# Optimization experiments

Measured on AMD Instinct MI355X. Metric: run time of the kernel, lower is better.

The kernel has to match this reference:

```python
import jax, jax.numpy as jnp
import numpy as np
import math

B, S, D, H = 4, 2048, 1024, 16
HD = D // H
EPS = 1e-10


def setup_inputs() -> dict:
    key = jax.random.key(0)
    kx, kq, kk, kv, ko = jax.random.split(key, 5)
    x = jax.random.normal(kx, (B, S, D), dtype=jnp.float32)
    # causal additive mask: 0 on/below diagonal, -1e9 above
    mask = jnp.where(jnp.triu(jnp.ones((S, S), dtype=bool), k=1), -1e9, 0.0).astype(jnp.float32)
    scale = 1.0 / math.sqrt(D)
    Wq = jax.random.normal(kq, (D, D), dtype=jnp.float32) * scale
    Wk = jax.random.normal(kk, (D, D), dtype=jnp.float32) * scale
    Wv = jax.random.normal(kv, (D, D), dtype=jnp.float32) * scale
    Wo = jax.random.normal(ko, (D, D), dtype=jnp.float32) * scale
    return {"x": x, "mask": mask, "Wq": Wq, "Wk": Wk, "Wv": Wv, "Wo": Wo}


def _nirmalya_softmax(t):
    # faithful to original: plain exp (no max-subtraction), eps in denominator
    p1 = jnp.exp(t)
    return p1 / (jnp.sum(p1, axis=-1, keepdims=True) + EPS)


def reference(x, mask, Wq, Wk, Wv, Wo):
    b, s, d = x.shape
    # torch Linear (bias=False): y = x @ W.T
    def proj(W):
        y = jnp.einsum('bsd,ed->bse', x, W)
        return y.reshape(b, s, H, HD).transpose(0, 2, 1, 3)  # [b,h,s,hd]
    q, k, v = proj(Wq), proj(Wk), proj(Wv)
    scores = jnp.einsum('bhqd,bhkd->bhqk', q, k) / math.sqrt(HD)
    scores = scores + mask  # broadcast over batch/heads
    attn = _nirmalya_softmax(scores)
    out = jnp.einsum('bhqk,bhkd->bhqd', attn, v)
    out = out.transpose(0, 2, 1, 3).reshape(b, s, d)
    return jnp.einsum('bsd,ed->bse', out, Wo)
```

## Files before the change

### kernel.cpp

```cpp
#include <hip/hip_runtime.h>
#include <hip/hip_bf16.h>

typedef __bf16 bf16;
typedef __attribute__((ext_vector_type(8))) __bf16 bf16x8;
typedef __attribute__((ext_vector_type(4))) float f32x4;

#define MFMA16(a, b, c) __builtin_amdgcn_mfma_f32_16x16x32_bf16((a), (b), (c), 0, 0, 0)

#define GLOAD_LDS16(gp, lp)                                                              \
  __builtin_amdgcn_global_load_lds(                                                      \
      (const __attribute__((address_space(1))) unsigned int*)(gp),                       \
      (__attribute__((address_space(3))) unsigned int*)(lp), 16, 0, 0)

#define BAR()   __builtin_amdgcn_s_barrier()
#define LGKM0() asm volatile("s_waitcnt lgkmcnt(0)" ::: "memory")
#define VMC(n)  asm volatile("s_waitcnt vmcnt(" #n ")" ::: "memory")
#define PRIO1() __builtin_amdgcn_s_setprio(1)
#define PRIO0() __builtin_amdgcn_s_setprio(0)

__global__ __launch_bounds__(256) void cvt_all(const float* __restrict__ x,
                                               const float* __restrict__ wq,
                                               const float* __restrict__ wk,
                                               const float* __restrict__ wv,
                                               const float* __restrict__ wo,
                                               bf16* __restrict__ xb,
                                               bf16* __restrict__ wqkv,
                                               bf16* __restrict__ wob) {
  constexpr int NXC = 8388608 / 8;
  constexpr int NWC = 1048576 / 8;
  constexpr int TOT = NXC + 4 * NWC;
  for (int c = blockIdx.x * 256 + threadIdx.x; c < TOT; c += gridDim.x * 256) {
    const float* src; bf16* dst; int idx;
    if (c < NXC) { src = x; dst = xb; idx = c; }
    else {
      int c2 = c - NXC; int wsel = c2 >> 17; idx = c2 & (NWC - 1);
      src = wsel == 0 ? wq : wsel == 1 ? wk : wsel == 2 ? wv : wo;
      dst = wsel < 3 ? wqkv + (size_t)wsel * 1048576 : wob;
    }
    float4 v0 = reinterpret_cast<const float4*>(src)[idx * 2];
    float4 v1 = reinterpret_cast<const float4*>(src)[idx * 2 + 1];
    bf16x8 o;
    o[0] = (bf16)v0.x; o[1] = (bf16)v0.y; o[2] = (bf16)v0.z; o[3] = (bf16)v0.w;
    o[4] = (bf16)v1.x; o[5] = (bf16)v1.y; o[6] = (bf16)v1.z; o[7] = (bf16)v1.w;
    reinterpret_cast<bf16x8*>(dst)[idx] = o;
  }
}

#define MMA8(BF, MH, NH)                                                                 \
  _Pragma("unroll") for (int mi = 0; mi < 2; ++mi)                                       \
  _Pragma("unroll") for (int ni = 0; ni < 2; ++ni)                                       \
  _Pragma("unroll") for (int ks = 0; ks < 2; ++ks)                                       \
      acc[(MH) * 2 + mi][(NH) * 2 + ni] =                                                \
          MFMA16(af[mi][ks], (BF)[ni][ks], acc[(MH) * 2 + mi][(NH) * 2 + ni]);

template <int MODE, int NT>
__global__ __launch_bounds__(512, 1) void gemm8(const bf16* __restrict__ A,
                                                const bf16* __restrict__ B,
                                                void* __restrict__ Cv,
                                                bf16* __restrict__ VT) {
  constexpr int K = 1024;
  __shared__ bf16 smem[49152];
  const int tid = threadIdx.x, lane = tid & 63, w = tid >> 6;
  const int l15 = lane & 15, l16 = lane >> 4;
  const int wr = w >> 2, wc = w & 3;
  const int lin = blockIdx.x;
  const int idx = lin >> 3;
  const int mt = (lin & 7) * 8 + idx / NT;
  const int nt = idx % NT;
  const int bm0 = mt * 128, bn0 = nt * 256;

  auto stA = [&](int buf, int t, int j) {
    const int r = j * 64 + (tid >> 3);
    const int g = (tid & 7) ^ (r & 7);
    GLOAD_LDS16(&A[(size_t)(bm0 + r) * K + t * 64 + g * 8],
                &smem[buf * 8192 + j * 4096 + tid * 8]);
  };
  auto stB = [&](int buf, int t, int j) {
    const int r = j * 64 + (tid >> 3);
    const int g = (tid & 7) ^ (r & 7);
    GLOAD_LDS16(&B[(size_t)(bn0 + r) * K + t * 64 + g * 8],
                &smem[16384 + buf * 16384 + j * 4096 + tid * 8]);
  };
  bf16x8 af[2][2], b0[2][2], b1[2][2];
  auto ldA = [&](int buf, int mh, bf16x8 (&dst)[2][2]) {
#pragma unroll
    for (int mi = 0; mi < 2; ++mi)
#pragma unroll
      for (int ks = 0; ks < 2; ++ks)
        dst[mi][ks] = *reinterpret_cast<const bf16x8*>(
            &smem[buf * 8192 + (wr * 64 + mh * 32 + mi * 16 + l15) * 64 +
                  (((ks * 4 + l16) ^ (l15 & 7)) * 8)]);
  };
  auto ldB = [&](int buf, int nh, bf16x8 (&dst)[2][2]) {
#pragma unroll
    for (int ni = 0; ni < 2; ++ni)
#pragma unroll
      for (int ks = 0; ks < 2; ++ks)
        dst[ni][ks] = *reinterpret_cast<const bf16x8*>(
            &smem[16384 + buf * 16384 + (wc * 64 + nh * 32 + ni * 16 + l15) * 64 +
                  (((ks * 4 + l16) ^ (l15 & 7)) * 8)]);
  };

  f32x4 acc[4][4] = {};

  stA(0, 0, 0); stA(0, 0, 1);
  stB(0, 0, 0); stB(0, 0, 1); stB(0, 0, 2); stB(0, 0, 3);
  stA(1, 1, 0); stA(1, 1, 1);
  stB(1, 1, 0); stB(1, 1, 1); stB(1, 1, 2); stB(1, 1, 3);
  VMC(6); BAR();

#pragma unroll 1
  for (int it = 0; it < K / 128; ++it) {
    const int t0 = 2 * it;
    const bool last = (it == K / 128 - 1);
    ldA(0, 0, af); ldB(0, 0, b0);
    BAR(); LGKM0();
    PRIO1(); MMA8(b0, 0, 0); PRIO0();
    BAR();
    ldB(0, 1, b1);
    BAR(); LGKM0();
    PRIO1(); MMA8(b1, 0, 1); PRIO0();
    BAR();
    ldA(0, 1, af);
    BAR(); LGKM0();
    PRIO1(); MMA8(b1, 1, 1); PRIO0();
    BAR();
    if (!last) {
      stA(0, t0 + 2, 0); stA(0, t0 + 2, 1);
      stB(0, t0 + 2, 0); stB(0, t0 + 2, 1); stB(0, t0 + 2, 2); stB(0, t0 + 2, 3);
    }
    PRIO1(); MMA8(b0, 1, 0); PRIO0();
    if (last) { VMC(0); } else { VMC(6); }
    BAR();
    ldA(1, 0, af); ldB(1, 0, b0);
    BAR(); LGKM0();
    PRIO1(); MMA8(b0, 0, 0); PRIO0();
    BAR();
    ldB(1, 1, b1);
    BAR(); LGKM0();
    PRIO1(); MMA8(b1, 0, 1); PRIO0();
    BAR();
    ldA(1, 1, af);
    BAR(); LGKM0();
    PRIO1(); MMA8(b1, 1, 1); PRIO0();
    BAR();
    if (!last) {
      stA(1, t0 + 3, 0); stA(1, t0 + 3, 1);
      stB(1, t0 + 3, 0); stB(1, t0 + 3, 1); stB(1, t0 + 3, 2); stB(1, t0 + 3, 3);
    }
    PRIO1(); MMA8(b0, 1, 0); PRIO0();
    if (!last) VMC(6);
    BAR();
  }

  if constexpr (MODE == 0) {
#pragma unroll
    for (int i = 0; i < 4; ++i)
#pragma unroll
      for (int j = 0; j < 4; ++j)
#pragma unroll
        for (int r = 0; r < 4; ++r) {
          const size_t row = bm0 + wr * 64 + (i >> 1) * 32 + (i & 1) * 16 + l16 * 4 + r;
          const size_t col = bn0 + wc * 64 + (j >> 1) * 32 + (j & 1) * 16 + l15;
          reinterpret_cast<float*>(Cv)[row * (NT * 256) + col] = acc[i][j][r];
        }
  } else {
    if (bn0 < 2048) {
#pragma unroll
      for (int i = 0; i < 4; ++i)
#pragma unroll
        for (int j = 0; j < 4; ++j)
#pragma unroll
          for (int r = 0; r < 4; ++r) {
            const size_t row = bm0 + wr * 64 + (i >> 1) * 32 + (i & 1) * 16 + l16 * 4 + r;
            const size_t col = bn0 + wc * 64 + (j >> 1) * 32 + (j & 1) * 16 + l15;
            reinterpret_cast<bf16*>(Cv)[row * 2048 + col] = (bf16)acc[i][j][r];
          }
    } else {
#pragma unroll
      for (int i = 0; i < 4; ++i)
#pragma unroll
        for (int j = 0; j < 4; ++j)
#pragma unroll
          for (int r = 0; r < 4; ++r) {
            const int m = wr * 64 + (i >> 1) * 32 + (i & 1) * 16 + l16 * 4 + r;
            const int n = wc * 64 + (j >> 1) * 32 + (j & 1) * 16 + l15;
            smem[n * 136 + m] = (bf16)acc[i][j][r];
          }
      BAR();
      const int n = tid >> 1, half = tid & 1;
      const size_t vbase = ((size_t)(bm0 >> 11) * 1024 + (bn0 - 2048 + n)) * 2048 +
                           (bm0 & 2047) + half * 64;
#pragma unroll
      for (int k = 0; k < 8; ++k) {
        bf16x8 v = *reinterpret_cast<const bf16x8*>(&smem[n * 136 + half * 64 + k * 8]);
        *reinterpret_cast<bf16x8*>(&VT[vbase + k * 8]) = v;
      }
    }
  }
}

constexpr int S_ = 2048, H_ = 16, LDQK = 2048;

__global__ __launch_bounds__(256, 4) void attn_kernel(const bf16* __restrict__ QK,
                                                      const bf16* __restrict__ VT,
                                                      bf16* __restrict__ AO) {
  __shared__ bf16 Ks[2][64 * 64];
  __shared__ bf16 Vs[2][64 * 64];
  __shared__ bf16 Ps[4][16 * 64];
  const int tid = threadIdx.x, lane = tid & 63, w = tid >> 6;
  const int l15 = lane & 15, l16 = lane >> 4;
  const int bh = blockIdx.x, b = bh >> 4, h = bh & (H_ - 1);
  const int pairid = blockIdx.y;
  const size_t qoff = (size_t)b * S_ * LDQK + h * 64;
  const size_t koff = qoff + 1024;
  const size_t voff = (size_t)bh * 64 * LDQK;
  const size_t aoff = (size_t)b * S_ * 1024 + h * 64;

  auto stage = [&](int t) {
    const int kv0 = t * 64, bs = t & 1;
#pragma unroll
    for (int i = 0; i < 2; ++i) {
      const int c = tid + 256 * i;
      const int row = c >> 3, gs = (c & 7) ^ (row & 7);
      GLOAD_LDS16(&QK[koff + (size_t)(kv0 + row) * LDQK + gs * 8], &Ks[bs][c * 8]);
      GLOAD_LDS16(&VT[voff + (size_t)row * LDQK + kv0 + gs * 8], &Vs[bs][c * 8]);
    }
  };

  const bf16 one_ = (bf16)1.0f;
  const bf16x8 ones = {one_, one_, one_, one_, one_, one_, one_, one_};

#pragma unroll 1
  for (int half = 0; half < 2; ++half) {
    const int j = half ? (31 - pairid) : pairid;
    const int qrow = j * 64 + w * 16;
    const int ntiles = j + 1;

    bf16x8 qf[2];
#pragma unroll
    for (int kk = 0; kk < 2; ++kk)
      qf[kk] = *reinterpret_cast<const bf16x8*>(
          &QK[qoff + (size_t)(qrow + l15) * LDQK + kk * 32 + l16 * 8]);

    f32x4 o[4] = {};
    f32x4 ors = {};

    stage(0);
    VMC(0); BAR();

#pragma unroll 1
    for (int t = 0; t < ntiles; ++t) {
      if (t + 1 < ntiles) stage(t + 1);
      const int bs = t & 1;
      f32x4 sc[4] = {};
#pragma unroll
      for (int kk = 0; kk < 2; ++kk) {
        bf16x8 kf[4];
#pragma unroll
        for (int ni = 0; ni < 4; ++ni)
          kf[ni] = *reinterpret_cast<bf16x8*>(
              &Ks[bs][(ni * 16 + l15) * 64 + (((kk * 4 + l16) ^ (l15 & 7)) * 8)]);
#pragma unroll
        for (int ni = 0; ni < 4; ++ni)
          sc[ni] = MFMA16(qf[kk], kf[ni], sc[ni]);
      }

      const bool diag = (t == j);
#pragma unroll
      for (int ni = 0; ni < 4; ++ni)
#pragma unroll
        for (int r = 0; r < 4; ++r) {
          const int lrow = l16 * 4 + r;
          const int lcol = ni * 16 + l15;
          float p = exp2f(sc[ni][r] * 0.18033688011112042f);
          if (diag) p = (lcol <= w * 16 + lrow) ? p : 0.0f;
          Ps[w][lrow * 64 + (lcol ^ ((lrow & 7) << 3))] = (bf16)p;
        }

#pragma unroll
      for (int kk = 0; kk < 2; ++kk) {
        bf16x8 pf = *reinterpret_cast<bf16x8*>(
            &Ps[w][l15 * 64 + (((kk * 4 + l16) ^ (l15 & 7)) * 8)]);
        bf16x8 vf[4];
#pragma unroll
        for (int ni = 0; ni < 4; ++ni)
          vf[ni] = *reinterpret_cast<bf16x8*>(
              &Vs[bs][(ni * 16 + l15) * 64 + (((kk * 4 + l16) ^ (l15 & 7)) * 8)]);
        ors = MFMA16(pf, ones, ors);
#pragma unroll
        for (int ni = 0; ni < 4; ++ni)
          o[ni] = MFMA16(pf, vf[ni], o[ni]);
      }
      VMC(0); BAR();
    }

#pragma unroll
    for (int ni = 0; ni < 4; ++ni)
#pragma unroll
      for (int r = 0; r < 4; ++r) {
        const int row = qrow + l16 * 4 + r;
        AO[aoff + (size_t)row * 1024 + ni * 16 + l15] =
            (bf16)(o[ni][r] / (ors[r] + 1e-10f));
      }
  }
}

extern "C" void kernel_launch(void* const* d_in, const int* in_sizes, int n_in,
                              void* d_out, int out_size, void* d_ws, size_t ws_size,
                              hipStream_t stream) {
  const float* x  = (const float*)d_in[0];
  const float* Wq = (const float*)d_in[2];
  const float* Wk = (const float*)d_in[3];
  const float* Wv = (const float*)d_in[4];
  const float* Wo = (const float*)d_in[5];

  constexpr int B = 4, S = 2048, D = 1024;
  constexpr size_t nx = (size_t)B * S * D;
  constexpr size_t nw = (size_t)D * D;

  char* ws = (char*)d_ws;
  bf16* xb    = (bf16*)ws;
  bf16* Wqkvb = xb + nx;
  bf16* Wob   = Wqkvb + 3 * nw;
  bf16* QKb   = Wob + nw;
  bf16* VTb   = QKb + (size_t)B * S * 2048;
  bf16* AOb   = VTb + nx;

  cvt_all<<<2048, 256, 0, stream>>>(x, Wq, Wk, Wv, Wo, xb, Wqkvb, Wob);

  gemm8<2, 12><<<768, 512, 0, stream>>>(xb, Wqkvb, QKb, VTb);

  attn_kernel<<<dim3(B * H_, 16), 256, 0, stream>>>(QKb, VTb, AOb);

  gemm8<0, 4><<<256, 512, 0, stream>>>(AOb, Wob, d_out, nullptr);
}
```

Baseline: 176.1 us.

## Give each attention wave 32 query rows with 2 waves per block

The attention kernel now uses 128-thread blocks in which each wave handles two 16-row query sub-tiles. Each K and V fragment read from LDS is therefore reused across twice as many MFMAs. The goal is to cut LDS read traffic per FLOP and improve the MFMA-to-load ratio. The costs are more accumulator registers, fewer waves per block to load each KV tile (4 loads per thread instead of 2), and possibly lower occupancy and less latency hiding.

```diff
diff --git a/kernel.cpp b/kernel.cpp
--- a/kernel.cpp
+++ b/kernel.cpp
@@ -202,12 +202,12 @@
 
 constexpr int S_ = 2048, H_ = 16, LDQK = 2048;
 
-__global__ __launch_bounds__(256, 4) void attn_kernel(const bf16* __restrict__ QK,
+__global__ __launch_bounds__(128, 2) void attn_kernel(const bf16* __restrict__ QK,
                                                       const bf16* __restrict__ VT,
                                                       bf16* __restrict__ AO) {
   __shared__ bf16 Ks[2][64 * 64];
   __shared__ bf16 Vs[2][64 * 64];
-  __shared__ bf16 Ps[4][16 * 64];
+  __shared__ bf16 Ps[2][32 * 64];
   const int tid = threadIdx.x, lane = tid & 63, w = tid >> 6;
   const int l15 = lane & 15, l16 = lane >> 4;
   const int bh = blockIdx.x, b = bh >> 4, h = bh & (H_ - 1);
@@ -220,8 +220,8 @@
   auto stage = [&](int t) {
     const int kv0 = t * 64, bs = t & 1;
 #pragma unroll
-    for (int i = 0; i < 2; ++i) {
-      const int c = tid + 256 * i;
+    for (int i = 0; i < 4; ++i) {
+      const int c = tid + 128 * i;
       const int row = c >> 3, gs = (c & 7) ^ (row & 7);
       GLOAD_LDS16(&QK[koff + (size_t)(kv0 + row) * LDQK + gs * 8], &Ks[bs][c * 8]);
       GLOAD_LDS16(&VT[voff + (size_t)row * LDQK + kv0 + gs * 8], &Vs[bs][c * 8]);
@@ -234,17 +234,19 @@
 #pragma unroll 1
   for (int half = 0; half < 2; ++half) {
     const int j = half ? (31 - pairid) : pairid;
-    const int qrow = j * 64 + w * 16;
+    const int qrow = j * 64 + w * 32;
     const int ntiles = j + 1;
 
-    bf16x8 qf[2];
-#pragma unroll
-    for (int kk = 0; kk < 2; ++kk)
-      qf[kk] = *reinterpret_cast<const bf16x8*>(
-          &QK[qoff + (size_t)(qrow + l15) * LDQK + kk * 32 + l16 * 8]);
-
-    f32x4 o[4] = {};
-    f32x4 ors = {};
+    bf16x8 qf[2][2];
+#pragma unroll
+    for (int mi = 0; mi < 2; ++mi)
+#pragma unroll
+      for (int kk = 0; kk < 2; ++kk)
+        qf[mi][kk] = *reinterpret_cast<const bf16x8*>(
+            &QK[qoff + (size_t)(qrow + mi * 16 + l15) * LDQK + kk * 32 + l16 * 8]);
+
+    f32x4 o[2][4] = {};
+    f32x4 ors[2] = {};
 
     stage(0);
     VMC(0); BAR();
@@ -253,7 +255,8 @@
     for (int t = 0; t < ntiles; ++t) {
       if (t + 1 < ntiles) stage(t + 1);
       const int bs = t & 1;
-      f32x4 sc[4] = {};
+      const int kv0 = t * 64;
+      f32x4 sc[2][4] = {};
 #pragma unroll
       for (int kk = 0; kk < 2; ++kk) {
         bf16x8 kf[4];
@@ -262,47 +265,59 @@
           kf[ni] = *reinterpret_cast<bf16x8*>(
               &Ks[bs][(ni * 16 + l15) * 64 + (((kk * 4 + l16) ^ (l15 & 7)) * 8)]);
 #pragma unroll
+        for (int mi = 0; mi < 2; ++mi)
+#pragma unroll
+          for (int ni = 0; ni < 4; ++ni)
+            sc[mi][ni] = MFMA16(qf[mi][kk], kf[ni], sc[mi][ni]);
+      }
+
+      const bool diag = (t == j);
+#pragma unroll
+      for (int mi = 0; mi < 2; ++mi)
+#pragma unroll
         for (int ni = 0; ni < 4; ++ni)
-          sc[ni] = MFMA16(qf[kk], kf[ni], sc[ni]);
-      }
-
-      const bool diag = (t == j);
-#pragma unroll
-      for (int ni = 0; ni < 4; ++ni)
-#pragma unroll
-        for (int r = 0; r < 4; ++r) {
-          const int lrow = l16 * 4 + r;
-          const int lcol = ni * 16 + l15;
-          float p = exp2f(sc[ni][r] * 0.18033688011112042f);
-          if (diag) p = (lcol <= w * 16 + lrow) ? p : 0.0f;
-          Ps[w][lrow * 64 + (lcol ^ ((lrow & 7) << 3))] = (bf16)p;
-        }
+#pragma unroll
+          for (int r = 0; r < 4; ++r) {
+            const int lrow = mi * 16 + l16 * 4 + r;
+            const int lcol = ni * 16 + l15;
+            float p = exp2f(sc[mi][ni][r] * 0.18033688011112042f);
+            if (diag) p = (kv0 + lcol <= qrow + lrow) ? p : 0.0f;
+            Ps[w][lrow * 64 + (lcol ^ ((lrow & 7) << 3))] = (bf16)p;
+          }
 
 #pragma unroll
       for (int kk = 0; kk < 2; ++kk) {
-        bf16x8 pf = *reinterpret_cast<bf16x8*>(
-            &Ps[w][l15 * 64 + (((kk * 4 + l16) ^ (l15 & 7)) * 8)]);
+        bf16x8 pf[2];
+#pragma unroll
+        for (int mi = 0; mi < 2; ++mi)
+          pf[mi] = *reinterpret_cast<bf16x8*>(
+              &Ps[w][(mi * 16 + l15) * 64 + (((kk * 4 + l16) ^ (l15 & 7)) * 8)]);
         bf16x8 vf[4];
 #pragma unroll
         for (int ni = 0; ni < 4; ++ni)
           vf[ni] = *reinterpret_cast<bf16x8*>(
               &Vs[bs][(ni * 16 + l15) * 64 + (((kk * 4 + l16) ^ (l15 & 7)) * 8)]);
-        ors = MFMA16(pf, ones, ors);
-#pragma unroll
-        for (int ni = 0; ni < 4; ++ni)
-          o[ni] = MFMA16(pf, vf[ni], o[ni]);
+#pragma unroll
+        for (int mi = 0; mi < 2; ++mi) {
+          ors[mi] = MFMA16(pf[mi], ones, ors[mi]);
+#pragma unroll
+          for (int ni = 0; ni < 4; ++ni)
+            o[mi][ni] = MFMA16(pf[mi], vf[ni], o[mi][ni]);
+        }
       }
       VMC(0); BAR();
     }
 
 #pragma unroll
-    for (int ni = 0; ni < 4; ++ni)
-#pragma unroll
-      for (int r = 0; r < 4; ++r) {
-        const int row = qrow + l16 * 4 + r;
-        AO[aoff + (size_t)row * 1024 + ni * 16 + l15] =
-            (bf16)(o[ni][r] / (ors[r] + 1e-10f));
-      }
+    for (int mi = 0; mi < 2; ++mi)
+#pragma unroll
+      for (int ni = 0; ni < 4; ++ni)
+#pragma unroll
+        for (int r = 0; r < 4; ++r) {
+          const int row = qrow + mi * 16 + l16 * 4 + r;
+          AO[aoff + (size_t)row * 1024 + ni * 16 + l15] =
+              (bf16)(o[mi][ni][r] / (ors[mi][r] + 1e-10f));
+        }
   }
 }
 
@@ -331,7 +346,7 @@
 
   gemm8<2, 12><<<768, 512, 0, stream>>>(xb, Wqkvb, QKb, VTb);
 
-  attn_kernel<<<dim3(B * H_, 16), 256, 0, stream>>>(QKb, VTb, AOb);
+  attn_kernel<<<dim3(B * H_, 16), 128, 0, stream>>>(QKb, VTb, AOb);
 
   gemm8<0, 4><<<256, 512, 0, stream>>>(AOb, Wob, d_out, nullptr);
 }
```

Result: slower. 182.9 us (+3.8%).

## Rewrite attention with 32x32 MFMA, register-resident P, and folded score scale

Applied to the files above, without the earlier changes.

The attention kernel now uses 128-thread blocks where each wave owns 32 query rows and computes S^T with 32x32x16 MFMAs. Probabilities are packed to bf16 in registers and exchanged with permlane32_swap instead of round-tripping through LDS. The row sum is accumulated on the VALU rather than with an extra MFMA against ones. The softmax scale is moved into the Q projection epilogue, and output is staged through LDS for coalesced 16-byte stores. The aims are to cut LDS traffic and redundant MFMA work, at the cost of fewer waves per block and changed occupancy.

```diff
diff --git a/kernel.cpp b/kernel.cpp
--- a/kernel.cpp
+++ b/kernel.cpp
@@ -4,8 +4,12 @@
 typedef __bf16 bf16;
 typedef __attribute__((ext_vector_type(8))) __bf16 bf16x8;
 typedef __attribute__((ext_vector_type(4))) float f32x4;
+typedef __attribute__((ext_vector_type(16))) float f32x16;
+typedef __attribute__((ext_vector_type(2))) unsigned int u32x2;
+typedef __attribute__((ext_vector_type(4))) unsigned int u32x4;
 
 #define MFMA16(a, b, c) __builtin_amdgcn_mfma_f32_16x16x32_bf16((a), (b), (c), 0, 0, 0)
+#define MFMA32(a, b, c) __builtin_amdgcn_mfma_f32_32x32x16_bf16((a), (b), (c), 0, 0, 0)
 
 #define GLOAD_LDS16(gp, lp)                                                              \
   __builtin_amdgcn_global_load_lds(                                                      \
@@ -174,7 +178,9 @@
           for (int r = 0; r < 4; ++r) {
             const size_t row = bm0 + wr * 64 + (i >> 1) * 32 + (i & 1) * 16 + l16 * 4 + r;
             const size_t col = bn0 + wc * 64 + (j >> 1) * 32 + (j & 1) * 16 + l15;
-            reinterpret_cast<bf16*>(Cv)[row * 2048 + col] = (bf16)acc[i][j][r];
+            float v = acc[i][j][r];
+            if (col < 1024) v *= 0.18033688011112042f;
+            reinterpret_cast<bf16*>(Cv)[row * 2048 + col] = (bf16)v;
           }
     } else {
 #pragma unroll
@@ -202,14 +208,14 @@
 
 constexpr int S_ = 2048, H_ = 16, LDQK = 2048;
 
-__global__ __launch_bounds__(256, 4) void attn_kernel(const bf16* __restrict__ QK,
+__global__ __launch_bounds__(128, 2) void attn_kernel(const bf16* __restrict__ QK,
                                                       const bf16* __restrict__ VT,
                                                       bf16* __restrict__ AO) {
   __shared__ bf16 Ks[2][64 * 64];
   __shared__ bf16 Vs[2][64 * 64];
-  __shared__ bf16 Ps[4][16 * 64];
   const int tid = threadIdx.x, lane = tid & 63, w = tid >> 6;
-  const int l15 = lane & 15, l16 = lane >> 4;
+  const int l31 = lane & 31, hi = lane >> 5;
+  const int x7 = l31 & 7;
   const int bh = blockIdx.x, b = bh >> 4, h = bh & (H_ - 1);
   const int pairid = blockIdx.y;
   const size_t qoff = (size_t)b * S_ * LDQK + h * 64;
@@ -220,31 +226,29 @@
   auto stage = [&](int t) {
     const int kv0 = t * 64, bs = t & 1;
 #pragma unroll
-    for (int i = 0; i < 2; ++i) {
-      const int c = tid + 256 * i;
+    for (int i = 0; i < 4; ++i) {
+      const int c = tid + 128 * i;
       const int row = c >> 3, gs = (c & 7) ^ (row & 7);
       GLOAD_LDS16(&QK[koff + (size_t)(kv0 + row) * LDQK + gs * 8], &Ks[bs][c * 8]);
       GLOAD_LDS16(&VT[voff + (size_t)row * LDQK + kv0 + gs * 8], &Vs[bs][c * 8]);
     }
   };
 
-  const bf16 one_ = (bf16)1.0f;
-  const bf16x8 ones = {one_, one_, one_, one_, one_, one_, one_, one_};
-
 #pragma unroll 1
   for (int half = 0; half < 2; ++half) {
     const int j = half ? (31 - pairid) : pairid;
-    const int qrow = j * 64 + w * 16;
+    const int qbase = j * 64 + w * 32;
     const int ntiles = j + 1;
-
-    bf16x8 qf[2];
-#pragma unroll
-    for (int kk = 0; kk < 2; ++kk)
-      qf[kk] = *reinterpret_cast<const bf16x8*>(
-          &QK[qoff + (size_t)(qrow + l15) * LDQK + kk * 32 + l16 * 8]);
-
-    f32x4 o[4] = {};
-    f32x4 ors = {};
+    const int qg = qbase + l31;
+
+    bf16x8 qf[4];
+#pragma unroll
+    for (int ks = 0; ks < 4; ++ks)
+      qf[ks] = *reinterpret_cast<const bf16x8*>(
+          &QK[qoff + (size_t)qg * LDQK + ks * 16 + hi * 8]);
+
+    f32x16 oT[2] = {};
+    float rs = 0.0f;
 
     stage(0);
     VMC(0); BAR();
@@ -253,56 +257,97 @@
     for (int t = 0; t < ntiles; ++t) {
       if (t + 1 < ntiles) stage(t + 1);
       const int bs = t & 1;
-      f32x4 sc[4] = {};
-#pragma unroll
-      for (int kk = 0; kk < 2; ++kk) {
-        bf16x8 kf[4];
-#pragma unroll
-        for (int ni = 0; ni < 4; ++ni)
-          kf[ni] = *reinterpret_cast<bf16x8*>(
-              &Ks[bs][(ni * 16 + l15) * 64 + (((kk * 4 + l16) ^ (l15 & 7)) * 8)]);
-#pragma unroll
-        for (int ni = 0; ni < 4; ++ni)
-          sc[ni] = MFMA16(qf[kk], kf[ni], sc[ni]);
+      const int kv0 = t * 64;
+
+      f32x16 sc[2] = {};
+      PRIO1();
+#pragma unroll
+      for (int ks = 0; ks < 4; ++ks) {
+        bf16x8 kf0 = *reinterpret_cast<bf16x8*>(
+            &Ks[bs][l31 * 64 + (((ks * 2 + hi) ^ x7) * 8)]);
+        bf16x8 kf1 = *reinterpret_cast<bf16x8*>(
+            &Ks[bs][(32 + l31) * 64 + (((ks * 2 + hi) ^ x7) * 8)]);
+        sc[0] = MFMA32(kf0, qf[ks], sc[0]);
+        sc[1] = MFMA32(kf1, qf[ks], sc[1]);
       }
+      PRIO0();
 
       const bool diag = (t == j);
-#pragma unroll
-      for (int ni = 0; ni < 4; ++ni)
-#pragma unroll
-        for (int r = 0; r < 4; ++r) {
-          const int lrow = l16 * 4 + r;
-          const int lcol = ni * 16 + l15;
-          float p = exp2f(sc[ni][r] * 0.18033688011112042f);
-          if (diag) p = (lcol <= w * 16 + lrow) ? p : 0.0f;
-          Ps[w][lrow * 64 + (lcol ^ ((lrow & 7) << 3))] = (bf16)p;
+      const int hi4 = hi * 4;
+#pragma unroll
+      for (int hh = 0; hh < 2; ++hh)
+#pragma unroll
+        for (int r = 0; r < 16; ++r) {
+          float e = exp2f(sc[hh][r]);
+          if (diag) {
+            const int kvg = kv0 + hh * 32 + (r & 3) + 8 * (r >> 2) + hi4;
+            e = (kvg <= qg) ? e : 0.0f;
+          }
+          rs += e;
+          sc[hh][r] = e;
         }
 
-#pragma unroll
-      for (int kk = 0; kk < 2; ++kk) {
-        bf16x8 pf = *reinterpret_cast<bf16x8*>(
-            &Ps[w][l15 * 64 + (((kk * 4 + l16) ^ (l15 & 7)) * 8)]);
-        bf16x8 vf[4];
-#pragma unroll
-        for (int ni = 0; ni < 4; ++ni)
-          vf[ni] = *reinterpret_cast<bf16x8*>(
-              &Vs[bs][(ni * 16 + l15) * 64 + (((kk * 4 + l16) ^ (l15 & 7)) * 8)]);
-        ors = MFMA16(pf, ones, ors);
-#pragma unroll
-        for (int ni = 0; ni < 4; ++ni)
-          o[ni] = MFMA16(pf, vf[ni], o[ni]);
+      u32x4 pf[4];
+#pragma unroll
+      for (int hh = 0; hh < 2; ++hh)
+#pragma unroll
+        for (int q4 = 0; q4 < 2; ++q4) {
+          unsigned x0, x1, y0, y1;
+          asm("v_cvt_pk_bf16_f32 %0, %1, %2" : "=v"(x0)
+              : "v"(sc[hh][q4 * 8 + 0]), "v"(sc[hh][q4 * 8 + 1]));
+          asm("v_cvt_pk_bf16_f32 %0, %1, %2" : "=v"(x1)
+              : "v"(sc[hh][q4 * 8 + 2]), "v"(sc[hh][q4 * 8 + 3]));
+          asm("v_cvt_pk_bf16_f32 %0, %1, %2" : "=v"(y0)
+              : "v"(sc[hh][q4 * 8 + 4]), "v"(sc[hh][q4 * 8 + 5]));
+          asm("v_cvt_pk_bf16_f32 %0, %1, %2" : "=v"(y1)
+              : "v"(sc[hh][q4 * 8 + 6]), "v"(sc[hh][q4 * 8 + 7]));
+          asm("v_permlane32_swap_b32 %0, %1" : "+v"(x0), "+v"(y0));
+          asm("v_permlane32_swap_b32 %0, %1" : "+v"(x1), "+v"(y1));
+          pf[hh * 2 + q4][0] = x0; pf[hh * 2 + q4][1] = x1;
+          pf[hh * 2 + q4][2] = y0; pf[hh * 2 + q4][3] = y1;
+        }
+
+      PRIO1();
+#pragma unroll
+      for (int ks = 0; ks < 4; ++ks) {
+        bf16x8 vt0 = *reinterpret_cast<bf16x8*>(
+            &Vs[bs][l31 * 64 + (((ks * 2 + hi) ^ x7) * 8)]);
+        bf16x8 vt1 = *reinterpret_cast<bf16x8*>(
+            &Vs[bs][(32 + l31) * 64 + (((ks * 2 + hi) ^ x7) * 8)]);
+        oT[0] = MFMA32(vt0, *reinterpret_cast<bf16x8*>(&pf[ks]), oT[0]);
+        oT[1] = MFMA32(vt1, *reinterpret_cast<bf16x8*>(&pf[ks]), oT[1]);
       }
+      PRIO0();
+
       VMC(0); BAR();
     }
 
-#pragma unroll
-    for (int ni = 0; ni < 4; ++ni)
-#pragma unroll
-      for (int r = 0; r < 4; ++r) {
-        const int row = qrow + l16 * 4 + r;
-        AO[aoff + (size_t)row * 1024 + ni * 16 + l15] =
-            (bf16)(o[ni][r] / (ors[r] + 1e-10f));
+    const float rst = rs + __shfl_xor(rs, 32);
+    const float inv = 1.0f / (rst + 1e-10f);
+
+    bf16* lo = &Ks[0][0] + w * 2048;
+#pragma unroll
+    for (int dh = 0; dh < 2; ++dh)
+#pragma unroll
+      for (int rq = 0; rq < 4; ++rq) {
+        const float v0 = oT[dh][rq * 4 + 0] * inv, v1 = oT[dh][rq * 4 + 1] * inv;
+        const float v2 = oT[dh][rq * 4 + 2] * inv, v3 = oT[dh][rq * 4 + 3] * inv;
+        unsigned d0, d1;
+        asm("v_cvt_pk_bf16_f32 %0, %1, %2" : "=v"(d0) : "v"(v0), "v"(v1));
+        asm("v_cvt_pk_bf16_f32 %0, %1, %2" : "=v"(d1) : "v"(v2), "v"(v3));
+        u32x2 dd; dd[0] = d0; dd[1] = d1;
+        *reinterpret_cast<u32x2*>(
+            &lo[l31 * 64 + (((dh * 4 + rq) ^ x7) * 8) + hi * 4]) = dd;
       }
+#pragma unroll
+    for (int jj = 0; jj < 4; ++jj) {
+      const int gran = lane + 64 * jj;
+      const int qr = gran >> 3, g = gran & 7;
+      bf16x8 vv = *reinterpret_cast<bf16x8*>(&lo[qr * 64 + ((g ^ (qr & 7)) * 8)]);
+      *reinterpret_cast<bf16x8*>(
+          &AO[aoff + (size_t)(j * 64 + w * 32 + qr) * 1024 + g * 8]) = vv;
+    }
+    LGKM0(); BAR();
   }
 }
 
@@ -331,7 +376,7 @@
 
   gemm8<2, 12><<<768, 512, 0, stream>>>(xb, Wqkvb, QKb, VTb);
 
-  attn_kernel<<<dim3(B * H_, 16), 256, 0, stream>>>(QKb, VTb, AOb);
+  attn_kernel<<<dim3(B * H_, 16), 128, 0, stream>>>(QKb, VTb, AOb);
 
   gemm8<0, 4><<<256, 512, 0, stream>>>(AOb, Wob, d_out, nullptr);
 }
```

Measured after the change: 174.6 us. Within noise of the previous version (-0.9%).
